# Performance work log

Measured on AMD Instinct MI355X. Metric: run time of the kernel, lower is better.

The kernel has to match this reference:

```python
import jax, jax.numpy as jnp
import numpy as np
from jax import lax

B, H, W_IN, C = 32, 32, 32, 128   # NHWC input
KH, KW = 3, 3                     # kernel size (padding 'same', stride 1)
F = 512                           # filters


def setup_inputs() -> dict:
    key = jax.random.key(0)
    ks = jax.random.split(key, 10)
    # sparse factor shapes: (KH*KW*C, 1152), (1152, F), (F, F)
    d0, d1, d2, d3 = KH * KW * C, 1152, F, F
    x = jax.random.normal(ks[0], (B, H, W_IN, C), dtype=jnp.float32)
    k0 = jax.random.normal(ks[1], (d0, d1), dtype=jnp.float32) * (1.0 / np.sqrt(d0))
    k1 = jax.random.normal(ks[2], (d1, d2), dtype=jnp.float32) * (1.0 / np.sqrt(d1))
    k2 = jax.random.normal(ks[3], (d2, d3), dtype=jnp.float32) * (1.0 / np.sqrt(d2))
    # fixed binary sparsity masks (K.constant in the original build)
    m0 = jax.random.bernoulli(ks[4], 0.1, (d0, d1)).astype(jnp.float32)
    m1 = jax.random.bernoulli(ks[5], 0.1, (d1, d2)).astype(jnp.float32)
    m2 = jax.random.bernoulli(ks[6], 0.1, (d2, d3)).astype(jnp.float32)
    scale = jax.random.normal(ks[7], (1,), dtype=jnp.float32)
    bias = jax.random.normal(ks[8], (F,), dtype=jnp.float32) * 0.01
    return {"x": x, "k0": k0, "k1": k1, "k2": k2,
            "m0": m0, "m1": m1, "m2": m2, "scale": scale, "bias": bias}


def reference(x, k0, k1, k2, m0, m1, m2, scale, bias):
    # Chained masked sparse factors collapse (associativity) to one effective
    # filter matrix of shape (KH*KW*C, F); the im2col row flatten order in the
    # original is (h, w, c), which matches an HWIO reshape exactly.
    w_eff = (k0 * m0) @ (k1 * m1) @ (k2 * m2)          # (KH*KW*C, F)
    w = (w_eff * scale[0]).reshape(KH, KW, C, F)        # fold scalar scale into kernel
    out = lax.conv_general_dilated(
        x, w, window_strides=(1, 1), padding='SAME',
        dimension_numbers=('NHWC', 'HWIO', 'NHWC'))     # (B, H, W, F)
    return out + bias
```

## Files before the change

### kernel.cpp

```cpp
#include <hip/hip_runtime.h>

typedef __attribute__((ext_vector_type(8))) short short8;
typedef __attribute__((ext_vector_type(4))) float f32x4;

typedef __attribute__((address_space(1))) const unsigned gas_u32;
typedef __attribute__((address_space(3))) unsigned las_u32;

static __device__ __forceinline__ void g2l16(const void* g, void* l) {
  __builtin_amdgcn_global_load_lds((gas_u32*)g, (las_u32*)l, 16, 0, 0);
}

static __device__ __forceinline__ short f2bf(float f) {
  union { float f; unsigned u; } v; v.f = f;
  unsigned r = (v.u + 0x7FFFu + ((v.u >> 16) & 1u)) >> 16;
  return (short)r;
}

#define MF(a_, b_, c_) __builtin_amdgcn_mfma_f32_16x16x32_bf16(a_, b_, c_, 0, 0, 0)

static __device__ __forceinline__ void maskmul8(const float* __restrict__ k,
                                                const float* __restrict__ m,
                                                float s, short* __restrict__ o8, int i) {
  const f32x4* kk = (const f32x4*)k + (size_t)i * 2;
  const f32x4* mm = (const f32x4*)m + (size_t)i * 2;
  f32x4 a0 = kk[0], a1 = kk[1], b0 = mm[0], b1 = mm[1];
  short8 o;
  o[0] = f2bf(a0[0] * b0[0] * s); o[1] = f2bf(a0[1] * b0[1] * s);
  o[2] = f2bf(a0[2] * b0[2] * s); o[3] = f2bf(a0[3] * b0[3] * s);
  o[4] = f2bf(a1[0] * b1[0] * s); o[5] = f2bf(a1[1] * b1[1] * s);
  o[6] = f2bf(a1[2] * b1[2] * s); o[7] = f2bf(a1[3] * b1[3] * s);
  ((short8*)o8)[i] = o;
}

static __device__ __forceinline__ void xcvt_body(const float* __restrict__ x,
                                                 short* __restrict__ xbp, int i) {
  int c8 = i & 15;
  int t = i >> 4;
  int wp = t % 34, t2 = t / 34;
  int hp = t2 % 34, b = t2 / 34;
  short8 o = {};
  if (hp >= 1 && hp <= 32 && wp >= 1 && wp <= 32) {
    const f32x4* s = (const f32x4*)(x + (((size_t)((b << 5) + hp - 1) << 5) + (wp - 1)) * 128 + c8 * 8);
    f32x4 a = s[0], bb2 = s[1];
    o[0] = f2bf(a[0]); o[1] = f2bf(a[1]); o[2] = f2bf(a[2]); o[3] = f2bf(a[3]);
    o[4] = f2bf(bb2[0]); o[5] = f2bf(bb2[1]); o[6] = f2bf(bb2[2]); o[7] = f2bf(bb2[3]);
  }
  ((short8*)xbp)[i] = o;
}

__global__ __launch_bounds__(256) void k_prep1(const float* __restrict__ k1f,
                                               const float* __restrict__ m1f,
                                               const float* __restrict__ k2f,
                                               const float* __restrict__ m2f,
                                               short* __restrict__ w2b,
                                               short* __restrict__ w3T,
                                               const float* __restrict__ x,
                                               short* __restrict__ xbp) {
  __shared__ float tile[32][33];
  const int bb = blockIdx.x, tid = threadIdx.x;
  if (bb < 288) {
    maskmul8(k1f, m1f, 1.0f, w2b, bb * 256 + tid);
  } else if (bb < 544) {
    const int idx = bb - 288;
    int f0 = (idx & 15) * 32, d0 = (idx >> 4) * 32;
    int tx = tid & 31, ty = tid >> 5;
#pragma unroll
    for (int i = 0; i < 4; ++i) {
      int d = d0 + ty + i * 8;
      size_t ix = (size_t)d * 512 + f0 + tx;
      tile[ty + i * 8][tx] = k2f[ix] * m2f[ix];
    }
    __syncthreads();
#pragma unroll
    for (int i = 0; i < 4; ++i) {
      int f = f0 + ty + i * 8;
      w3T[(size_t)f * 512 + d0 + tx] = f2bf(tile[tx][ty + i * 8]);
    }
  } else {
    xcvt_body(x, xbp, (bb - 544) * 256 + tid);
  }
}

__global__ __launch_bounds__(256) void k_gemmx(const short* __restrict__ A,
                                               const short* __restrict__ BT,
                                               short* __restrict__ C, int M, int N, int K,
                                               const float* __restrict__ x,
                                               short* __restrict__ xbp, int xoff,
                                               const float* __restrict__ mkf,
                                               const float* __restrict__ mmf,
                                               const float* __restrict__ mscf,
                                               short* __restrict__ mout, int nmask) {
  __shared__ __align__(16) short As[2][64][128];
  __shared__ __align__(16) short Bs[2][64][128];
  if (blockIdx.x >= 144) {
    const int r = (int)blockIdx.x - 144;
    if (r < nmask) maskmul8(mkf, mmf, mscf[0], mout, r * 256 + (int)threadIdx.x);
    else xcvt_body(x, xbp, (xoff + r - nmask) * 256 + (int)threadIdx.x);
    return;
  }
  const int ntiles = N >> 6;
  const int m0 = (blockIdx.x / ntiles) << 6, n0 = (blockIdx.x % ntiles) << 6;
  const int tid = threadIdx.x;
  const int lane = tid & 63, wv = tid >> 6;
  const int wr = (wv >> 1) * 32, wc = (wv & 1) * 32;
  const int lr = lane & 15, lh = lane >> 4;

  const int rr = tid >> 4, sl = tid & 15;
  const int swz = sl ^ (rr & 7);
  const unsigned aOff = (unsigned)(m0 + rr) * K + swz * 8;
  const unsigned bOff = (unsigned)(n0 + rr) * K + swz * 8;
  const int ldsRow = 4 * wv;

  f32x4 acc[2][2] = {};

#define GST(buf_, kt_) do { \
    _Pragma("unroll") for (int j = 0; j < 4; ++j) \
      g2l16(A + aOff + (unsigned)j * 16u * (unsigned)K + (unsigned)(kt_) * 128u, \
            &As[buf_][j * 16 + ldsRow][0]); \
    _Pragma("unroll") for (int j = 0; j < 4; ++j) \
      g2l16(BT + bOff + (unsigned)j * 16u * (unsigned)K + (unsigned)(kt_) * 128u, \
            &Bs[buf_][j * 16 + ldsRow][0]); \
  } while (0)

  const int nk = K >> 7;
  GST(0, 0);
  asm volatile("s_waitcnt vmcnt(0)" ::: "memory");
  __builtin_amdgcn_s_barrier();

  for (int kt = 0; kt < nk; ++kt) {
    const int cur = kt & 1;
    if (kt + 1 < nk) { if (cur) GST(0, kt + 1); else GST(1, kt + 1); }
#pragma unroll
    for (int ks = 0; ks < 4; ++ks) {
      short8 af[2], bf[2];
#pragma unroll
      for (int i = 0; i < 2; ++i)
        af[i] = *(const short8*)&As[cur][wr + i * 16 + lr][((ks * 4 + lh) ^ (lr & 7)) * 8];
#pragma unroll
      for (int i = 0; i < 2; ++i)
        bf[i] = *(const short8*)&Bs[cur][wc + i * 16 + lr][((ks * 4 + lh) ^ (lr & 7)) * 8];
#pragma unroll
      for (int mi = 0; mi < 2; ++mi)
#pragma unroll
        for (int ni = 0; ni < 2; ++ni)
          acc[mi][ni] = MF(af[mi], bf[ni], acc[mi][ni]);
    }
    if (kt + 1 < nk) asm volatile("s_waitcnt vmcnt(0)" ::: "memory");
    __builtin_amdgcn_s_barrier();
  }
#pragma unroll
  for (int mi = 0; mi < 2; ++mi) {
    const int row = m0 + wr + mi * 16 + lh * 4;
#pragma unroll
    for (int ni = 0; ni < 2; ++ni) {
      const int col = n0 + wc + ni * 16 + lr;
#pragma unroll
      for (int q = 0; q < 4; ++q)
        C[(size_t)(row + q) * N + col] = f2bf(acc[mi][ni][q]);
    }
  }
#undef GST
}

#define RD_A(mf_, ks_) \
  (*(const short8*)&As[wr * 128 + (mf_) * 16 + lr][(((ks_) * 4 + lh) ^ (lr & 7)) * 8])
#define RD_B(nf_, ks_) \
  (*(const short8*)&Bs[wc * 64 + (nf_) * 16 + lr][(((ks_) * 4 + lh) ^ (lr & 7)) * 8])

#define STAGE_AQ(q_, tt_) do { \
  const int tc_ = (tt_) > 17 ? 17 : (tt_); \
  const int khw_ = tc_ >> 1; const int kh_ = (khw_ * 11) >> 5; const int kw_ = khw_ - kh_ * 3; \
  const int ao_ = (kh_ * 34 + kw_) * 128 + ((tc_ & 1) << 6) + (q_) * 4352; \
  g2l16(xbp + aBase + ao_, &As[(q_) * 32 + ldsA][0]); \
  g2l16(xbp + aBase + 17408 + ao_, &As[128 + (q_) * 32 + ldsA][0]); } while (0)

#define STAGE_B(tt_) do { \
  const int tc_ = (tt_) > 17 ? 17 : (tt_); \
  g2l16(wT + bBase +          tc_ * 64, &Bs[     ldsA][0]); \
  g2l16(wT + bBase +  36864 + tc_ * 64, &Bs[32 + ldsA][0]); \
  g2l16(wT + bBase +  73728 + tc_ * 64, &Bs[64 + ldsA][0]); \
  g2l16(wT + bBase + 110592 + tc_ * 64, &Bs[96 + ldsA][0]); } while (0)

#define MFMA16(p_) \
  acc[2*(p_)  ][0] = MF(a0k0, bfr[0][0], acc[2*(p_)  ][0]); \
  acc[2*(p_)  ][1] = MF(a0k0, bfr[1][0], acc[2*(p_)  ][1]); \
  acc[2*(p_)  ][2] = MF(a0k0, bfr[2][0], acc[2*(p_)  ][2]); \
  acc[2*(p_)  ][3] = MF(a0k0, bfr[3][0], acc[2*(p_)  ][3]); \
  acc[2*(p_)+1][0] = MF(a1k0, bfr[0][0], acc[2*(p_)+1][0]); \
  acc[2*(p_)+1][1] = MF(a1k0, bfr[1][0], acc[2*(p_)+1][1]); \
  acc[2*(p_)+1][2] = MF(a1k0, bfr[2][0], acc[2*(p_)+1][2]); \
  acc[2*(p_)+1][3] = MF(a1k0, bfr[3][0], acc[2*(p_)+1][3]); \
  acc[2*(p_)  ][0] = MF(a0k1, bfr[0][1], acc[2*(p_)  ][0]); \
  acc[2*(p_)  ][1] = MF(a0k1, bfr[1][1], acc[2*(p_)  ][1]); \
  acc[2*(p_)  ][2] = MF(a0k1, bfr[2][1], acc[2*(p_)  ][2]); \
  acc[2*(p_)  ][3] = MF(a0k1, bfr[3][1], acc[2*(p_)  ][3]); \
  acc[2*(p_)+1][0] = MF(a1k1, bfr[0][1], acc[2*(p_)+1][0]); \
  acc[2*(p_)+1][1] = MF(a1k1, bfr[1][1], acc[2*(p_)+1][1]); \
  acc[2*(p_)+1][2] = MF(a1k1, bfr[2][1], acc[2*(p_)+1][2]); \
  acc[2*(p_)+1][3] = MF(a1k1, bfr[3][1], acc[2*(p_)+1][3]);

#define PHASE(p_, PRE, WAITV, ...) do { \
  PRE; \
  short8 a0k0 = RD_A(2*(p_), 0),   a0k1 = RD_A(2*(p_), 1); \
  short8 a1k0 = RD_A(2*(p_)+1, 0), a1k1 = RD_A(2*(p_)+1, 1); \
  __VA_ARGS__ \
  asm volatile("s_waitcnt lgkmcnt(0)" ::: "memory"); \
  __builtin_amdgcn_sched_barrier(0); \
  __builtin_amdgcn_s_setprio(1); \
  MFMA16(p_) \
  __builtin_amdgcn_s_setprio(0); \
  WAITV; \
  __builtin_amdgcn_s_barrier(); \
} while (0)

#define LOADB do { \
  bfr[0][0] = RD_B(0, 0); bfr[0][1] = RD_B(0, 1); \
  bfr[1][0] = RD_B(1, 0); bfr[1][1] = RD_B(1, 1); \
  bfr[2][0] = RD_B(2, 0); bfr[2][1] = RD_B(2, 1); \
  bfr[3][0] = RD_B(3, 0); bfr[3][1] = RD_B(3, 1); } while (0)

#define VM4 asm volatile("s_waitcnt vmcnt(4)" ::: "memory")
#define VM6 asm volatile("s_waitcnt vmcnt(6)" ::: "memory")
#define VM8 asm volatile("s_waitcnt vmcnt(8)" ::: "memory")

__global__ __launch_bounds__(256, 2) void k_conv(const short* __restrict__ xbp,
                                                 const short* __restrict__ wT,
                                                 const float* __restrict__ bias,
                                                 float* __restrict__ outp) {
  __shared__ __align__(16) short As[256][64];
  __shared__ __align__(16) short Bs[128][64];
  int bid = blockIdx.x;
  bid = (bid & 7) * 64 + (bid >> 3);
  const int mt = bid >> 2, nt = bid & 3;
  const int m0 = mt << 8, n0 = nt << 7;
  const int tid = threadIdx.x;
  const int lane = tid & 63, wid = tid >> 6;
  const int wr = wid >> 1, wc = wid & 1;
  const int lr = lane & 15, lh = lane >> 4;

  f32x4 acc[8][4] = {};
  short8 bfr[4][2];

  const int rsub = tid >> 3;
  const int sw = (tid & 7) ^ (rsub & 7);
  const int ldsA = wid * 8;

  const int Mb = m0 + rsub;
  const int b = Mb >> 10, h0 = (Mb >> 5) & 31, w = Mb & 31;
  const unsigned aBase = (unsigned)((b * 34 + h0) * 34 + w) * 128 + sw * 8;
  const unsigned bBase = (unsigned)(n0 + rsub) * 1152 + sw * 8;

  STAGE_B(0);
  STAGE_AQ(0, 0); STAGE_AQ(1, 0); STAGE_AQ(2, 0);
  asm volatile("s_waitcnt vmcnt(0)" ::: "memory");
  __builtin_amdgcn_s_barrier();

  for (int t = 0; t < 18; ++t) {
    const int tn = t + 1;
    PHASE(0, LOADB, VM4, STAGE_AQ(3, t););
    PHASE(1, ,      VM6, STAGE_B(tn););
    PHASE(2, ,      VM8, STAGE_AQ(0, tn); STAGE_AQ(1, tn););
    PHASE(3, ,      VM4, STAGE_AQ(2, tn););
  }
  asm volatile("s_waitcnt vmcnt(0)" ::: "memory");

  const int orow = m0 + wr * 128, ocol = n0 + wc * 64;
#pragma unroll
  for (int mf = 0; mf < 8; ++mf) {
    const int row = orow + mf * 16 + lh * 4;
#pragma unroll
    for (int nf = 0; nf < 4; ++nf) {
      const int col = ocol + nf * 16 + lr;
      const float bv = bias[col];
#pragma unroll
      for (int q = 0; q < 4; ++q)
        outp[(size_t)(row + q) * 512 + col] = acc[mf][nf][q] + bv;
    }
  }
}

extern "C" void kernel_launch(void* const* d_in, const int* in_sizes, int n_in,
                              void* d_out, int out_size, void* d_ws, size_t ws_size,
                              hipStream_t stream) {
  (void)in_sizes; (void)n_in; (void)out_size; (void)ws_size;
  const float* x    = (const float*)d_in[0];
  const float* k0   = (const float*)d_in[1];
  const float* k1   = (const float*)d_in[2];
  const float* k2   = (const float*)d_in[3];
  const float* m0   = (const float*)d_in[4];
  const float* m1   = (const float*)d_in[5];
  const float* m2   = (const float*)d_in[6];
  const float* sc   = (const float*)d_in[7];
  const float* bias = (const float*)d_in[8];
  float* outp = (float*)d_out;
  char* ws = (char*)d_ws;

  short* xbp = (short*)(ws);
  short* w1b = (short*)(ws + 9469952);
  short* w2b = (short*)(ws + 12124160);
  short* w3T = (short*)(ws + 13303808);
  short* B1T = (short*)(ws + 13828096);
  short* wET = (short*)(ws + 15007744);

  k_prep1<<<1568, 256, 0, stream>>>(k1, m1, k2, m2, w2b, w3T, x, xbp);
  k_gemmx<<<1304, 256, 0, stream>>>(w3T, w2b, B1T, 512, 1152, 512,
                                    x, xbp, 1024, k0, m0, sc, w1b, 648);
  k_gemmx<<<920, 256, 0, stream>>>(B1T, w1b, wET, 512, 1152, 1152,
                                   x, xbp, 1536, (const float*)nullptr,
                                   (const float*)nullptr, (const float*)nullptr,
                                   (short*)nullptr, 0);
  k_conv<<<512, 256, 0, stream>>>(xbp, wET, bias, outp);
}
```

Baseline: 69.22 us.

## Fuse prep and two weight GEMMs into one persistent kernel with grid barriers

Replaces the three launches (prep, GEMM1, GEMM2) with one 256-block persistent kernel. Its phases are separated by software grid barriers built on per-block flags and an epoch counter kept in the workspace. This removes launch gaps and per-kernel tail effects, at the cost of fewer blocks doing the mask and convert work serially. It also relies on all 256 blocks being co-resident, which is needed to avoid deadlock.

```diff
diff --git a/kernel.cpp b/kernel.cpp
--- a/kernel.cpp
+++ b/kernel.cpp
@@ -48,59 +48,15 @@
   ((short8*)xbp)[i] = o;
 }
 
-__global__ __launch_bounds__(256) void k_prep1(const float* __restrict__ k1f,
-                                               const float* __restrict__ m1f,
-                                               const float* __restrict__ k2f,
-                                               const float* __restrict__ m2f,
-                                               short* __restrict__ w2b,
-                                               short* __restrict__ w3T,
-                                               const float* __restrict__ x,
-                                               short* __restrict__ xbp) {
-  __shared__ float tile[32][33];
-  const int bb = blockIdx.x, tid = threadIdx.x;
-  if (bb < 288) {
-    maskmul8(k1f, m1f, 1.0f, w2b, bb * 256 + tid);
-  } else if (bb < 544) {
-    const int idx = bb - 288;
-    int f0 = (idx & 15) * 32, d0 = (idx >> 4) * 32;
-    int tx = tid & 31, ty = tid >> 5;
-#pragma unroll
-    for (int i = 0; i < 4; ++i) {
-      int d = d0 + ty + i * 8;
-      size_t ix = (size_t)d * 512 + f0 + tx;
-      tile[ty + i * 8][tx] = k2f[ix] * m2f[ix];
-    }
-    __syncthreads();
-#pragma unroll
-    for (int i = 0; i < 4; ++i) {
-      int f = f0 + ty + i * 8;
-      w3T[(size_t)f * 512 + d0 + tx] = f2bf(tile[tx][ty + i * 8]);
-    }
-  } else {
-    xcvt_body(x, xbp, (bb - 544) * 256 + tid);
-  }
-}
-
-__global__ __launch_bounds__(256) void k_gemmx(const short* __restrict__ A,
-                                               const short* __restrict__ BT,
-                                               short* __restrict__ C, int M, int N, int K,
-                                               const float* __restrict__ x,
-                                               short* __restrict__ xbp, int xoff,
-                                               const float* __restrict__ mkf,
-                                               const float* __restrict__ mmf,
-                                               const float* __restrict__ mscf,
-                                               short* __restrict__ mout, int nmask) {
-  __shared__ __align__(16) short As[2][64][128];
-  __shared__ __align__(16) short Bs[2][64][128];
-  if (blockIdx.x >= 144) {
-    const int r = (int)blockIdx.x - 144;
-    if (r < nmask) maskmul8(mkf, mmf, mscf[0], mout, r * 256 + (int)threadIdx.x);
-    else xcvt_body(x, xbp, (xoff + r - nmask) * 256 + (int)threadIdx.x);
-    return;
-  }
+static __device__ __forceinline__ void gemm_tile(const short* __restrict__ A,
+                                                 const short* __restrict__ BT,
+                                                 short* __restrict__ C,
+                                                 int M, int N, int K, int tile,
+                                                 char* smem, int tid) {
+  short (*As)[64][128] = (short(*)[64][128])smem;
+  short (*Bs)[64][128] = (short(*)[64][128])(smem + 32768);
   const int ntiles = N >> 6;
-  const int m0 = (blockIdx.x / ntiles) << 6, n0 = (blockIdx.x % ntiles) << 6;
-  const int tid = threadIdx.x;
+  const int m0 = (tile / ntiles) << 6, n0 = (tile % ntiles) << 6;
   const int lane = tid & 63, wv = tid >> 6;
   const int wr = (wv >> 1) * 32, wc = (wv & 1) * 32;
   const int lr = lane & 15, lh = lane >> 4;
@@ -113,7 +69,7 @@
 
   f32x4 acc[2][2] = {};
 
-#define GST(buf_, kt_) do { \
+#define GSTm(buf_, kt_) do { \
     _Pragma("unroll") for (int j = 0; j < 4; ++j) \
       g2l16(A + aOff + (unsigned)j * 16u * (unsigned)K + (unsigned)(kt_) * 128u, \
             &As[buf_][j * 16 + ldsRow][0]); \
@@ -123,13 +79,13 @@
   } while (0)
 
   const int nk = K >> 7;
-  GST(0, 0);
+  GSTm(0, 0);
   asm volatile("s_waitcnt vmcnt(0)" ::: "memory");
-  __builtin_amdgcn_s_barrier();
+  __syncthreads();
 
   for (int kt = 0; kt < nk; ++kt) {
     const int cur = kt & 1;
-    if (kt + 1 < nk) { if (cur) GST(0, kt + 1); else GST(1, kt + 1); }
+    if (kt + 1 < nk) { if (cur) GSTm(0, kt + 1); else GSTm(1, kt + 1); }
 #pragma unroll
     for (int ks = 0; ks < 4; ++ks) {
       short8 af[2], bf[2];
@@ -146,7 +102,7 @@
           acc[mi][ni] = MF(af[mi], bf[ni], acc[mi][ni]);
     }
     if (kt + 1 < nk) asm volatile("s_waitcnt vmcnt(0)" ::: "memory");
-    __builtin_amdgcn_s_barrier();
+    __syncthreads();
   }
 #pragma unroll
   for (int mi = 0; mi < 2; ++mi) {
@@ -159,7 +115,93 @@
         C[(size_t)(row + q) * N + col] = f2bf(acc[mi][ni][q]);
     }
   }
-#undef GST
+#undef GSTm
+}
+
+static __device__ __forceinline__ void gbar(unsigned* flags, unsigned tag, int bid, int tid) {
+  __syncthreads();
+  if (tid == 0) {
+    __threadfence();
+    __hip_atomic_store(&flags[bid], tag, __ATOMIC_RELEASE, __HIP_MEMORY_SCOPE_AGENT);
+  }
+  while (__hip_atomic_load(&flags[tid], __ATOMIC_ACQUIRE, __HIP_MEMORY_SCOPE_AGENT) != tag)
+    __builtin_amdgcn_s_sleep(1);
+  __threadfence();
+  __syncthreads();
+}
+
+__global__ __launch_bounds__(256) void k_mega(const float* __restrict__ k0f,
+                                              const float* __restrict__ m0f,
+                                              const float* __restrict__ scf,
+                                              const float* __restrict__ k1f,
+                                              const float* __restrict__ m1f,
+                                              const float* __restrict__ k2f,
+                                              const float* __restrict__ m2f,
+                                              const float* __restrict__ x,
+                                              short* __restrict__ xbp,
+                                              short* __restrict__ w1b,
+                                              short* __restrict__ w2b,
+                                              short* __restrict__ w3T,
+                                              short* __restrict__ B1T,
+                                              short* __restrict__ wET,
+                                              unsigned* __restrict__ flags) {
+  __shared__ __align__(16) char smem[65536];
+  const int bid = blockIdx.x, tid = threadIdx.x;
+  const unsigned E = __hip_atomic_load(&flags[256], __ATOMIC_RELAXED, __HIP_MEMORY_SCOPE_AGENT);
+
+  float (*tile)[33] = (float(*)[33])smem;
+#pragma unroll 1
+  for (int j = 0; j < 8; ++j) {
+    const int u = j * 256 + bid;
+    if (u < 288) {
+      maskmul8(k1f, m1f, 1.0f, w2b, u * 256 + tid);
+    } else if (u < 544) {
+      const int idx = u - 288;
+      int f0 = (idx & 15) * 32, d0 = (idx >> 4) * 32;
+      int tx = tid & 31, ty = tid >> 5;
+      __syncthreads();
+#pragma unroll
+      for (int i = 0; i < 4; ++i) {
+        int d = d0 + ty + i * 8;
+        size_t ix = (size_t)d * 512 + f0 + tx;
+        tile[ty + i * 8][tx] = k2f[ix] * m2f[ix];
+      }
+      __syncthreads();
+#pragma unroll
+      for (int i = 0; i < 4; ++i) {
+        int f = f0 + ty + i * 8;
+        w3T[(size_t)f * 512 + d0 + tx] = f2bf(tile[tx][ty + i * 8]);
+      }
+    } else {
+      xcvt_body(x, xbp, (u - 544) * 256 + tid);
+    }
+  }
+  gbar(flags, E + 1, bid, tid);
+
+  if (bid < 144) {
+    gemm_tile(w3T, w2b, B1T, 512, 1152, 512, bid, smem, tid);
+  } else {
+    const int ab = bid - 144;
+#pragma unroll 1
+    for (int j = 0; j < 9; ++j) {
+      const int s = ab * 9 + j;
+      if (s < 648) maskmul8(k0f, m0f, scf[0], w1b, s * 256 + tid);
+      else xcvt_body(x, xbp, (1504 + s - 648) * 256 + tid);
+    }
+  }
+  gbar(flags, E + 2, bid, tid);
+
+  if (bid < 144) {
+    gemm_tile(B1T, w1b, wET, 512, 1152, 1152, bid, smem, tid);
+  } else {
+    const int ab = bid - 144;
+#pragma unroll 1
+    for (int j = 0; j < 4; ++j)
+      xcvt_body(x, xbp, (1864 + ab * 4 + j) * 256 + tid);
+  }
+
+  if (bid == 0 && tid == 0)
+    __hip_atomic_store(&flags[256], E + 2, __ATOMIC_RELAXED, __HIP_MEMORY_SCOPE_AGENT);
 }
 
 #define RD_A(mf_, ks_) \
@@ -295,19 +337,15 @@
   float* outp = (float*)d_out;
   char* ws = (char*)d_ws;
 
-  short* xbp = (short*)(ws);
-  short* w1b = (short*)(ws + 9469952);
-  short* w2b = (short*)(ws + 12124160);
-  short* w3T = (short*)(ws + 13303808);
-  short* B1T = (short*)(ws + 13828096);
-  short* wET = (short*)(ws + 15007744);
-
-  k_prep1<<<1568, 256, 0, stream>>>(k1, m1, k2, m2, w2b, w3T, x, xbp);
-  k_gemmx<<<1304, 256, 0, stream>>>(w3T, w2b, B1T, 512, 1152, 512,
-                                    x, xbp, 1024, k0, m0, sc, w1b, 648);
-  k_gemmx<<<920, 256, 0, stream>>>(B1T, w1b, wET, 512, 1152, 1152,
-                                   x, xbp, 1536, (const float*)nullptr,
-                                   (const float*)nullptr, (const float*)nullptr,
-                                   (short*)nullptr, 0);
+  short* xbp   = (short*)(ws);
+  short* w1b   = (short*)(ws + 9469952);
+  short* w2b   = (short*)(ws + 12124160);
+  short* w3T   = (short*)(ws + 13303808);
+  short* B1T   = (short*)(ws + 13828096);
+  short* wET   = (short*)(ws + 15007744);
+  unsigned* fl = (unsigned*)(ws + 16187392);
+
+  k_mega<<<256, 256, 0, stream>>>(k0, m0, sc, k1, m1, k2, m2, x, xbp,
+                                  w1b, w2b, w3T, B1T, wET, fl);
   k_conv<<<512, 256, 0, stream>>>(xbp, wET, bias, outp);
 }
```

Result: slower. 160.4 us (+131.7%).
